# Kernel tuning notes

Measured on AMD Instinct MI355X. Metric: run time of the kernel, lower is better.

## Reference

```python
import jax, jax.numpy as jnp
import numpy as np

NUM_HEADS = 16

def setup_inputs() -> dict:
    key = jax.random.key(0)
    ks = jax.random.split(key, 7)
    B, N, C, R = 2, 2048, 1024, 64
    s = lambda fan_in: 1.0 / np.sqrt(fan_in)
    return {
        "x": jax.random.normal(ks[0], (B, N, C), dtype=jnp.float32),
        "w_qkv_a": jax.random.uniform(ks[1], (C, R), jnp.float32, -s(C), s(C)),
        "w_qkv_b": jax.random.uniform(ks[2], (R, 3 * C), jnp.float32, -s(R), s(R)),
        "w_proj_a": jax.random.uniform(ks[3], (C, R), jnp.float32, -s(C), s(C)),
        "b_proj_a": jax.random.uniform(ks[4], (R,), jnp.float32, -s(C), s(C)),
        "w_proj_b": jax.random.uniform(ks[5], (R, C), jnp.float32, -s(R), s(R)),
        "b_proj_b": jax.random.uniform(ks[6], (C,), jnp.float32, -s(R), s(R)),
    }

def reference(x, w_qkv_a, w_qkv_b, w_proj_a, b_proj_a, w_proj_b, b_proj_b):
    B, N, C = x.shape
    H = NUM_HEADS
    Dh = C // H
    scale = Dh ** -0.5
    # LoRA QKV: dim -> rank -> 3*dim with exact GELU between (no bias, qkv_bias=False)
    qkv = jax.nn.gelu(x @ w_qkv_a, approximate=False) @ w_qkv_b  # [B,N,3C]
    qkv = qkv.reshape(B, N, 3, H, Dh).transpose(2, 0, 3, 1, 4)  # [3,B,H,N,Dh]
    q, k, v = qkv[0] * scale, qkv[1], qkv[2]
    attn = jax.nn.softmax(jnp.einsum("bhqd,bhkd->bhqk", q, k), axis=-1)
    out = jnp.einsum("bhqk,bhkd->bhqd", attn, v)  # [B,H,N,Dh]
    out = out.transpose(0, 2, 1, 3).reshape(B, N, C)
    # LoRA proj: dim -> rank -> dim with bias (proj_bias=True)
    out = jax.nn.gelu(out @ w_proj_a + b_proj_a, approximate=False) @ w_proj_b + b_proj_b
    return out
```

## Files before the change

### kernel.cpp

```cpp
#include <hip/hip_runtime.h>
#include <cstdint>
#include <cstddef>


typedef short short8 __attribute__((ext_vector_type(8)));
typedef float f32x4 __attribute__((ext_vector_type(4)));
typedef __fp16 half2v __attribute__((ext_vector_type(2)));
typedef __fp16 half4 __attribute__((ext_vector_type(4)));

#define MFMA16(a, b, c) __builtin_amdgcn_mfma_f32_16x16x32_bf16((a), (b), (c), 0, 0, 0)
#define MFMA16F(a, b, c) __builtin_amdgcn_mfma_f32_16x16x16f16((a), (b), (c), 0, 0, 0)

#define QSCALE 0.18033688011112042f

__device__ __forceinline__ float fexp2(float x) { return __builtin_amdgcn_exp2f(x); }

__device__ __forceinline__ uint16_t f2b(float f) {
    return (uint16_t)((__float_as_uint(f) + 0x8000u) >> 16);
}
__device__ __forceinline__ uint32_t pkbf(float a, float b) {
    uint32_t ua = __float_as_uint(a) + 0x8000u;
    uint32_t ub = __float_as_uint(b) + 0x8000u;
    return __builtin_amdgcn_perm(ub, ua, 0x07060302);
}
__device__ __forceinline__ uint16_t f2h(float f) {
    half2v t = __builtin_amdgcn_cvt_pkrtz(f, f);
    return __builtin_bit_cast(uint16_t, t[0]);
}
__device__ __forceinline__ float gelu_exact(float x) {
    return 0.5f * x * (1.0f + erff(x * 0.70710678118654752440f));
}
__device__ __forceinline__ short8 ld8(const uint16_t* p) {
    return *reinterpret_cast<const short8*>(p);
}

__global__ __launch_bounds__(256) void prep(const float* __restrict__ x,
                                            const float* __restrict__ wqa,
                                            const float* __restrict__ wqb,
                                            const float* __restrict__ wpa,
                                            const float* __restrict__ wpb,
                                            uint16_t* __restrict__ xb,
                                            uint16_t* __restrict__ wqaT,
                                            uint16_t* __restrict__ wqbT,
                                            uint16_t* __restrict__ wpaT,
                                            uint16_t* __restrict__ wpbT) {
    const int bid = blockIdx.x;
    if (bid < 2048) {
        size_t i = ((size_t)bid * 256 + threadIdx.x) * 8;
        f32x4 a0 = *reinterpret_cast<const f32x4*>(x + i);
        f32x4 a1 = *reinterpret_cast<const f32x4*>(x + i + 4);
        uint32_t* o = reinterpret_cast<uint32_t*>(xb + i);
        o[0] = pkbf(a0[0], a0[1]);
        o[1] = pkbf(a0[2], a0[3]);
        o[2] = pkbf(a1[0], a1[1]);
        o[3] = pkbf(a1[2], a1[3]);
        return;
    }
    int i = (bid - 2048) * 256 + threadIdx.x;
    if (i < 65536) {
        int r = i >> 6, c = i & 63;
        wqaT[(size_t)c * 1024 + r] = f2b(wqa[i]);
    } else if (i < 262144) {
        int j = i - 65536;
        int r = j / 3072, c = j - r * 3072;
        wqbT[(size_t)c * 64 + r] = f2b(wqb[j]);
    } else if (i < 327680) {
        int j = i - 262144;
        int r = j >> 6, c = j & 63;
        wpaT[(size_t)c * 1024 + r] = f2b(wpa[j]);
    } else {
        int j = i - 327680;
        int r = j >> 10, c = j & 1023;
        wpbT[(size_t)c * 64 + r] = f2b(wpb[j]);
    }
}

__global__ __launch_bounds__(512) void rank_gemm(const uint16_t* __restrict__ X,
                                                 const uint16_t* __restrict__ WT,
                                                 const float* __restrict__ bias,
                                                 uint16_t* __restrict__ out) {
    __shared__ float ps[4][16][17];
    const int tid = threadIdx.x;
    const int wave = tid >> 6, lane = tid & 63;
    const int l16 = lane & 15, quad = lane >> 4;
    const int cc = wave & 3, kh = wave >> 2;
    const int rowg = blockIdx.x;

    const uint16_t* ap = X + (size_t)(rowg * 16 + l16) * 1024 + kh * 512 + quad * 8;
    const uint16_t* bp = WT + (size_t)(cc * 16 + l16) * 1024 + kh * 512 + quad * 8;

    f32x4 acc = {0.f, 0.f, 0.f, 0.f};
#pragma unroll 8
    for (int k = 0; k < 16; ++k) {
        acc = MFMA16(ld8(ap + k * 32), ld8(bp + k * 32), acc);
    }

    if (kh == 1) {
#pragma unroll
        for (int r = 0; r < 4; ++r) ps[cc][quad * 4 + r][l16] = acc[r];
    }
    __syncthreads();
    if (kh == 0) {
        const int col = cc * 16 + l16;
        const float bv = bias ? bias[col] : 0.0f;
#pragma unroll
        for (int r = 0; r < 4; ++r) {
            int row = rowg * 16 + quad * 4 + r;
            float v = acc[r] + ps[cc][quad * 4 + r][l16] + bv;
            out[(size_t)row * 64 + col] = f2b(gelu_exact(v));
        }
    }
}

__global__ __launch_bounds__(256) void expand_qkv(const uint16_t* __restrict__ H1,
                                                  const uint16_t* __restrict__ WT,
                                                  uint16_t* __restrict__ Qb,
                                                  uint16_t* __restrict__ Kb,
                                                  uint16_t* __restrict__ Vb) {
    __shared__ __align__(16) uint16_t po[4][16 * 72];
    const int wave = threadIdx.x >> 6;
    const int lane = threadIdx.x & 63;
    const int l16 = lane & 15, quad = lane >> 4;
    const int wg = blockIdx.x * 4 + wave;
    const int rowg = wg / 48;
    const int colg = wg % 48;

    const uint16_t* ap = H1 + (size_t)(rowg * 16 + l16) * 64 + quad * 8;
    const uint16_t* bp = WT + ((size_t)colg * 64 + l16) * 64 + quad * 8;

    f32x4 acc[4];
#pragma unroll
    for (int c = 0; c < 4; ++c) acc[c] = (f32x4){0.f, 0.f, 0.f, 0.f};

#pragma unroll
    for (int i = 0; i < 2; ++i) {
        short8 a = ld8(ap + i * 32);
#pragma unroll
        for (int c = 0; c < 4; ++c) {
            acc[c] = MFMA16(a, ld8(bp + (size_t)c * 16 * 64 + i * 32), acc[c]);
        }
    }

    const int which = colg >> 4;
    const int h = colg & 15;
    uint16_t* pw = po[wave];
#pragma unroll
    for (int c = 0; c < 4; ++c) {
#pragma unroll
        for (int r = 0; r < 4; ++r) {
            float v = acc[c][r];
            uint16_t u = (which == 0) ? f2b(v * QSCALE)
                       : (which == 1) ? f2b(v) : f2h(v);
            pw[(quad * 4 + r) * 72 + c * 16 + l16] = u;
        }
    }
    __builtin_amdgcn_s_waitcnt(0);

    const int grow = rowg * 16 + l16;
    const int b = grow >> 11, n = grow & 2047;
    uint16_t* base = (which == 0) ? Qb : (which == 1) ? Kb : Vb;
    uint16_t* dst = base + ((size_t)(b * 16 + h) * 2048 + n) * 64 + quad * 16;
    *reinterpret_cast<short8*>(dst) = ld8(&pw[l16 * 72 + quad * 16]);
    *reinterpret_cast<short8*>(dst + 8) = ld8(&pw[l16 * 72 + quad * 16 + 8]);
}

__global__ __launch_bounds__(256) void vtrans(const uint16_t* __restrict__ Vb,
                                              uint16_t* __restrict__ Vtb) {
    __shared__ __align__(16) uint16_t tl[64 * 72];
    const int bh = blockIdx.x >> 5;
    const int nt = blockIdx.x & 31;
    const int r = threadIdx.x >> 2;
    const int c0 = (threadIdx.x & 3) << 4;

    const uint16_t* g = Vb + ((size_t)(bh * 2048 + nt * 64 + r)) * 64 + c0;
    union { short8 v; uint16_t u[8]; } a0, a1;
    a0.v = ld8(g);
    a1.v = ld8(g + 8);
#pragma unroll
    for (int j = 0; j < 8; ++j) {
        tl[(c0 + j) * 72 + r] = a0.u[j];
        tl[(c0 + 8 + j) * 72 + r] = a1.u[j];
    }
    __syncthreads();
    uint16_t* o = Vtb + ((size_t)(bh * 64 + r)) * 2048 + nt * 64 + c0;
    *reinterpret_cast<short8*>(o) = ld8(&tl[r * 72 + c0]);
    *reinterpret_cast<short8*>(o + 8) = ld8(&tl[r * 72 + c0 + 8]);
}

__global__ __launch_bounds__(256) void attn_kernel(const uint16_t* __restrict__ Qb,
                                                   const uint16_t* __restrict__ Kb,
                                                   const uint16_t* __restrict__ Vtb,
                                                   uint16_t* __restrict__ AO) {
    __shared__ __align__(16) uint16_t kt[64 * 72];
    __shared__ __align__(16) uint16_t vt[64 * 72];

    const int tid = threadIdx.x;
    const int wave = tid >> 6;
    const int lane = tid & 63;
    const int l16 = lane & 15, quad = lane >> 4;
    const int bh = blockIdx.x >> 5;
    const int qg = blockIdx.x & 31;
    const int q16 = qg * 64 + wave * 16;

    const uint16_t* qp = Qb + ((size_t)(bh * 2048 + q16 + l16)) * 64 + quad * 8;
    const short8 qf0 = ld8(qp);
    const short8 qf1 = ld8(qp + 32);

    f32x4 ot[4];
#pragma unroll
    for (int dc = 0; dc < 4; ++dc) ot[dc] = (f32x4){0.f, 0.f, 0.f, 0.f};
    float lp = 0.f;

    const int sr = tid >> 2;
    const int sc = (tid & 3) << 4;

    for (int t = 0; t < 32; ++t) {
        __syncthreads();
        {
            const uint16_t* kg = Kb + ((size_t)(bh * 2048 + t * 64 + sr)) * 64 + sc;
            *reinterpret_cast<short8*>(&kt[sr * 72 + sc]) = ld8(kg);
            *reinterpret_cast<short8*>(&kt[sr * 72 + sc + 8]) = ld8(kg + 8);
            const uint16_t* vg = Vtb + ((size_t)(bh * 64 + sr)) * 2048 + t * 64 + sc;
            *reinterpret_cast<short8*>(&vt[sr * 72 + sc]) = ld8(vg);
            *reinterpret_cast<short8*>(&vt[sr * 72 + sc + 8]) = ld8(vg + 8);
        }
        __syncthreads();

        half4 pb[4];
#pragma unroll
        for (int kc = 0; kc < 4; ++kc) {
            const uint16_t* kp = &kt[(kc * 16 + l16) * 72 + quad * 8];
            f32x4 st = {0.f, 0.f, 0.f, 0.f};
            st = MFMA16(ld8(kp), qf0, st);
            st = MFMA16(ld8(kp + 32), qf1, st);
            float p0 = fexp2(st[0]), p1 = fexp2(st[1]);
            float p2 = fexp2(st[2]), p3 = fexp2(st[3]);
            lp += (p0 + p1) + (p2 + p3);
            half2v lo = __builtin_amdgcn_cvt_pkrtz(p0, p1);
            half2v hi = __builtin_amdgcn_cvt_pkrtz(p2, p3);
            pb[kc] = __builtin_shufflevector(lo, hi, 0, 1, 2, 3);
        }

#pragma unroll
        for (int dc = 0; dc < 4; ++dc) {
#pragma unroll
            for (int kc = 0; kc < 4; ++kc) {
                const half4 av = *reinterpret_cast<const half4*>(
                    vt + (dc * 16 + l16) * 72 + kc * 16 + quad * 4);
                ot[dc] = MFMA16F(av, pb[kc], ot[dc]);
            }
        }
    }

    lp += __shfl_xor(lp, 16, 64);
    lp += __shfl_xor(lp, 32, 64);
    const float inv = 1.0f / lp;

    __syncthreads();
    uint16_t* pw = &kt[wave * 1152];
#pragma unroll
    for (int dc = 0; dc < 4; ++dc) {
        uint32_t* w = reinterpret_cast<uint32_t*>(&pw[l16 * 72 + dc * 16 + quad * 4]);
        w[0] = pkbf(ot[dc][0] * inv, ot[dc][1] * inv);
        w[1] = pkbf(ot[dc][2] * inv, ot[dc][3] * inv);
    }
    __builtin_amdgcn_s_waitcnt(0);

    const int b = bh >> 4, h = bh & 15;
    const int grow = b * 2048 + q16 + l16;
    uint16_t* dst = AO + (size_t)grow * 1024 + h * 64 + quad * 16;
    *reinterpret_cast<short8*>(dst) = ld8(&pw[l16 * 72 + quad * 16]);
    *reinterpret_cast<short8*>(dst + 8) = ld8(&pw[l16 * 72 + quad * 16 + 8]);
}

__global__ __launch_bounds__(256) void expand_out(const uint16_t* __restrict__ H2,
                                                  const uint16_t* __restrict__ WT,
                                                  const float* __restrict__ bias,
                                                  float* __restrict__ out) {
    const int wave = threadIdx.x >> 6;
    const int lane = threadIdx.x & 63;
    const int l16 = lane & 15, quad = lane >> 4;
    const int wg = blockIdx.x * 4 + wave;
    const int rowg = wg >> 4;
    const int colg = wg & 15;

    const uint16_t* ap = H2 + (size_t)(rowg * 16 + l16) * 64 + quad * 8;
    const uint16_t* bp = WT + ((size_t)colg * 64 + l16) * 64 + quad * 8;

    f32x4 acc[4];
#pragma unroll
    for (int c = 0; c < 4; ++c) acc[c] = (f32x4){0.f, 0.f, 0.f, 0.f};

#pragma unroll
    for (int i = 0; i < 2; ++i) {
        short8 a = ld8(ap + i * 32);
#pragma unroll
        for (int c = 0; c < 4; ++c) {
            acc[c] = MFMA16(a, ld8(bp + (size_t)c * 16 * 64 + i * 32), acc[c]);
        }
    }

#pragma unroll
    for (int c = 0; c < 4; ++c) {
        int col = colg * 64 + c * 16 + l16;
        float bv = bias[col];
#pragma unroll
        for (int r = 0; r < 4; ++r) {
            int row = rowg * 16 + quad * 4 + r;
            out[(size_t)row * 1024 + col] = acc[c][r] + bv;
        }
    }
}

extern "C" void kernel_launch(void* const* d_in, const int* in_sizes, int n_in,
                              void* d_out, int out_size, void* d_ws, size_t ws_size,
                              hipStream_t stream) {
    const float* x   = (const float*)d_in[0];
    const float* wqa = (const float*)d_in[1];
    const float* wqb = (const float*)d_in[2];
    const float* wpa = (const float*)d_in[3];
    const float* bpa = (const float*)d_in[4];
    const float* wpb = (const float*)d_in[5];
    const float* bpb = (const float*)d_in[6];
    float* out = (float*)d_out;
    uint16_t* ws = (uint16_t*)d_ws;

    uint16_t* wqaT = ws + 0;
    uint16_t* wqbT = ws + 65536;
    uint16_t* wpaT = ws + 262144;
    uint16_t* wpbT = ws + 327680;
    uint16_t* h1   = ws + 393216;
    uint16_t* Qb   = ws + 655360;
    uint16_t* Kb   = ws + 4849664;
    uint16_t* xb   = Kb;
    uint16_t* Vtb  = ws + 9043968;
    uint16_t* AO   = ws + 13238272;
    uint16_t* Vb   = AO;
    uint16_t* h2   = ws + 17432576;
    (void)in_sizes; (void)n_in; (void)out_size; (void)ws_size;

    prep<<<3584, 256, 0, stream>>>(x, wqa, wqb, wpa, wpb, xb, wqaT, wqbT, wpaT, wpbT);
    rank_gemm<<<256, 512, 0, stream>>>(xb, wqaT, nullptr, h1);
    expand_qkv<<<3072, 256, 0, stream>>>(h1, wqbT, Qb, Kb, Vb);
    vtrans<<<1024, 256, 0, stream>>>(Vb, Vtb);
    attn_kernel<<<1024, 256, 0, stream>>>(Qb, Kb, Vtb, AO);
    rank_gemm<<<256, 512, 0, stream>>>(AO, wpaT, bpa, h2);
    expand_out<<<1024, 256, 0, stream>>>(h2, wpbT, bpb, out);
}
```

Baseline: 205.2 us.

## Fuse V transpose into QKV expand, read K/V directly, fuse projection GEMMs

The V transpose kernel is removed: expand_qkv now computes V^T by swapping the MFMA operands and writes it straight into the transposed layout with scalar strided stores. The attention kernel drops LDS staging and the per-tile barriers for K and V, loading MFMA fragments directly from global memory and relying on cache reuse across waves. The two projection kernels are merged into one, which keeps the rank-64 GELU activation in LDS. This removes two launches and intermediate round trips, at the risk of uncoalesced 2-byte V stores and redundant global loads of K and V in attention.

```diff
diff --git a/kernel.cpp b/kernel.cpp
--- a/kernel.cpp
+++ b/kernel.cpp
@@ -77,7 +77,6 @@
 
 __global__ __launch_bounds__(512) void rank_gemm(const uint16_t* __restrict__ X,
                                                  const uint16_t* __restrict__ WT,
-                                                 const float* __restrict__ bias,
                                                  uint16_t* __restrict__ out) {
     __shared__ float ps[4][16][17];
     const int tid = threadIdx.x;
@@ -102,11 +101,10 @@
     __syncthreads();
     if (kh == 0) {
         const int col = cc * 16 + l16;
-        const float bv = bias ? bias[col] : 0.0f;
 #pragma unroll
         for (int r = 0; r < 4; ++r) {
             int row = rowg * 16 + quad * 4 + r;
-            float v = acc[r] + ps[cc][quad * 4 + r][l16] + bv;
+            float v = acc[r] + ps[cc][quad * 4 + r][l16];
             out[(size_t)row * 64 + col] = f2b(gelu_exact(v));
         }
     }
@@ -116,7 +114,7 @@
                                                   const uint16_t* __restrict__ WT,
                                                   uint16_t* __restrict__ Qb,
                                                   uint16_t* __restrict__ Kb,
-                                                  uint16_t* __restrict__ Vb) {
+                                                  uint16_t* __restrict__ Vtb) {
     __shared__ __align__(16) uint16_t po[4][16 * 72];
     const int wave = threadIdx.x >> 6;
     const int lane = threadIdx.x & 63;
@@ -128,71 +126,69 @@
     const uint16_t* ap = H1 + (size_t)(rowg * 16 + l16) * 64 + quad * 8;
     const uint16_t* bp = WT + ((size_t)colg * 64 + l16) * 64 + quad * 8;
 
-    f32x4 acc[4];
-#pragma unroll
-    for (int c = 0; c < 4; ++c) acc[c] = (f32x4){0.f, 0.f, 0.f, 0.f};
-
-#pragma unroll
-    for (int i = 0; i < 2; ++i) {
-        short8 a = ld8(ap + i * 32);
-#pragma unroll
-        for (int c = 0; c < 4; ++c) {
-            acc[c] = MFMA16(a, ld8(bp + (size_t)c * 16 * 64 + i * 32), acc[c]);
-        }
-    }
-
     const int which = colg >> 4;
     const int h = colg & 15;
-    uint16_t* pw = po[wave];
-#pragma unroll
-    for (int c = 0; c < 4; ++c) {
-#pragma unroll
-        for (int r = 0; r < 4; ++r) {
-            float v = acc[c][r];
-            uint16_t u = (which == 0) ? f2b(v * QSCALE)
-                       : (which == 1) ? f2b(v) : f2h(v);
-            pw[(quad * 4 + r) * 72 + c * 16 + l16] = u;
-        }
-    }
-    __builtin_amdgcn_s_waitcnt(0);
-
-    const int grow = rowg * 16 + l16;
-    const int b = grow >> 11, n = grow & 2047;
-    uint16_t* base = (which == 0) ? Qb : (which == 1) ? Kb : Vb;
-    uint16_t* dst = base + ((size_t)(b * 16 + h) * 2048 + n) * 64 + quad * 16;
-    *reinterpret_cast<short8*>(dst) = ld8(&pw[l16 * 72 + quad * 16]);
-    *reinterpret_cast<short8*>(dst + 8) = ld8(&pw[l16 * 72 + quad * 16 + 8]);
-}
-
-__global__ __launch_bounds__(256) void vtrans(const uint16_t* __restrict__ Vb,
-                                              uint16_t* __restrict__ Vtb) {
-    __shared__ __align__(16) uint16_t tl[64 * 72];
-    const int bh = blockIdx.x >> 5;
-    const int nt = blockIdx.x & 31;
-    const int r = threadIdx.x >> 2;
-    const int c0 = (threadIdx.x & 3) << 4;
-
-    const uint16_t* g = Vb + ((size_t)(bh * 2048 + nt * 64 + r)) * 64 + c0;
-    union { short8 v; uint16_t u[8]; } a0, a1;
-    a0.v = ld8(g);
-    a1.v = ld8(g + 8);
-#pragma unroll
-    for (int j = 0; j < 8; ++j) {
-        tl[(c0 + j) * 72 + r] = a0.u[j];
-        tl[(c0 + 8 + j) * 72 + r] = a1.u[j];
-    }
-    __syncthreads();
-    uint16_t* o = Vtb + ((size_t)(bh * 64 + r)) * 2048 + nt * 64 + c0;
-    *reinterpret_cast<short8*>(o) = ld8(&tl[r * 72 + c0]);
-    *reinterpret_cast<short8*>(o + 8) = ld8(&tl[r * 72 + c0 + 8]);
+
+    f32x4 acc[4];
+#pragma unroll
+    for (int c = 0; c < 4; ++c) acc[c] = (f32x4){0.f, 0.f, 0.f, 0.f};
+
+    if (which < 2) {
+#pragma unroll
+        for (int i = 0; i < 2; ++i) {
+            short8 a = ld8(ap + i * 32);
+#pragma unroll
+            for (int c = 0; c < 4; ++c) {
+                acc[c] = MFMA16(a, ld8(bp + (size_t)c * 1024 + i * 32), acc[c]);
+            }
+        }
+        uint16_t* pw = po[wave];
+#pragma unroll
+        for (int c = 0; c < 4; ++c) {
+#pragma unroll
+            for (int r = 0; r < 4; ++r) {
+                float v = acc[c][r];
+                uint16_t u = (which == 0) ? f2b(v * QSCALE) : f2b(v);
+                pw[(quad * 4 + r) * 72 + c * 16 + l16] = u;
+            }
+        }
+        __builtin_amdgcn_s_waitcnt(0);
+
+        const int grow = rowg * 16 + l16;
+        const int b = grow >> 11, n = grow & 2047;
+        uint16_t* base = (which == 0) ? Qb : Kb;
+        uint16_t* dst = base + ((size_t)(b * 16 + h) * 2048 + n) * 64 + quad * 16;
+        *reinterpret_cast<short8*>(dst) = ld8(&pw[l16 * 72 + quad * 16]);
+        *reinterpret_cast<short8*>(dst + 8) = ld8(&pw[l16 * 72 + quad * 16 + 8]);
+    } else {
+#pragma unroll
+        for (int i = 0; i < 2; ++i) {
+            short8 a = ld8(ap + i * 32);
+#pragma unroll
+            for (int c = 0; c < 4; ++c) {
+                acc[c] = MFMA16(ld8(bp + (size_t)c * 1024 + i * 32), a, acc[c]);
+            }
+        }
+        const int grow = rowg * 16 + l16;
+        const int b = grow >> 11, n = grow & 2047;
+        uint16_t* vb = Vtb + (size_t)(b * 16 + h) * 64 * 2048 + n;
+#pragma unroll
+        for (int c = 0; c < 4; ++c) {
+#pragma unroll
+            for (int r = 0; r < 4; ++r) {
+                int d = c * 16 + quad * 4 + r;
+                vb[(size_t)d * 2048] = f2h(acc[c][r]);
+            }
+            vb += 0;
+        }
+    }
 }
 
 __global__ __launch_bounds__(256) void attn_kernel(const uint16_t* __restrict__ Qb,
                                                    const uint16_t* __restrict__ Kb,
                                                    const uint16_t* __restrict__ Vtb,
                                                    uint16_t* __restrict__ AO) {
-    __shared__ __align__(16) uint16_t kt[64 * 72];
-    __shared__ __align__(16) uint16_t vt[64 * 72];
+    __shared__ __align__(16) uint16_t pws[4][16 * 72];
 
     const int tid = threadIdx.x;
     const int wave = tid >> 6;
@@ -206,30 +202,19 @@
     const short8 qf0 = ld8(qp);
     const short8 qf1 = ld8(qp + 32);
 
+    const uint16_t* kbase = Kb + (size_t)bh * 2048 * 64 + (size_t)l16 * 64 + quad * 8;
+    const uint16_t* vbase = Vtb + (size_t)bh * 64 * 2048 + (size_t)l16 * 2048 + quad * 4;
+
     f32x4 ot[4];
 #pragma unroll
     for (int dc = 0; dc < 4; ++dc) ot[dc] = (f32x4){0.f, 0.f, 0.f, 0.f};
     float lp = 0.f;
 
-    const int sr = tid >> 2;
-    const int sc = (tid & 3) << 4;
-
     for (int t = 0; t < 32; ++t) {
-        __syncthreads();
-        {
-            const uint16_t* kg = Kb + ((size_t)(bh * 2048 + t * 64 + sr)) * 64 + sc;
-            *reinterpret_cast<short8*>(&kt[sr * 72 + sc]) = ld8(kg);
-            *reinterpret_cast<short8*>(&kt[sr * 72 + sc + 8]) = ld8(kg + 8);
-            const uint16_t* vg = Vtb + ((size_t)(bh * 64 + sr)) * 2048 + t * 64 + sc;
-            *reinterpret_cast<short8*>(&vt[sr * 72 + sc]) = ld8(vg);
-            *reinterpret_cast<short8*>(&vt[sr * 72 + sc + 8]) = ld8(vg + 8);
-        }
-        __syncthreads();
-
         half4 pb[4];
 #pragma unroll
         for (int kc = 0; kc < 4; ++kc) {
-            const uint16_t* kp = &kt[(kc * 16 + l16) * 72 + quad * 8];
+            const uint16_t* kp = kbase + (size_t)(t * 64 + kc * 16) * 64;
             f32x4 st = {0.f, 0.f, 0.f, 0.f};
             st = MFMA16(ld8(kp), qf0, st);
             st = MFMA16(ld8(kp + 32), qf1, st);
@@ -243,10 +228,10 @@
 
 #pragma unroll
         for (int dc = 0; dc < 4; ++dc) {
+            const uint16_t* vp = vbase + (size_t)dc * 16 * 2048 + t * 64;
 #pragma unroll
             for (int kc = 0; kc < 4; ++kc) {
-                const half4 av = *reinterpret_cast<const half4*>(
-                    vt + (dc * 16 + l16) * 72 + kc * 16 + quad * 4);
+                const half4 av = *reinterpret_cast<const half4*>(vp + kc * 16);
                 ot[dc] = MFMA16F(av, pb[kc], ot[dc]);
             }
         }
@@ -256,8 +241,7 @@
     lp += __shfl_xor(lp, 32, 64);
     const float inv = 1.0f / lp;
 
-    __syncthreads();
-    uint16_t* pw = &kt[wave * 1152];
+    uint16_t* pw = pws[wave];
 #pragma unroll
     for (int dc = 0; dc < 4; ++dc) {
         uint32_t* w = reinterpret_cast<uint32_t*>(&pw[l16 * 72 + dc * 16 + quad * 4]);
@@ -273,41 +257,59 @@
     *reinterpret_cast<short8*>(dst + 8) = ld8(&pw[l16 * 72 + quad * 16 + 8]);
 }
 
-__global__ __launch_bounds__(256) void expand_out(const uint16_t* __restrict__ H2,
-                                                  const uint16_t* __restrict__ WT,
-                                                  const float* __restrict__ bias,
+__global__ __launch_bounds__(512) void proj_fused(const uint16_t* __restrict__ AO,
+                                                  const uint16_t* __restrict__ wpaT,
+                                                  const float* __restrict__ bpa,
+                                                  const uint16_t* __restrict__ wpbT,
+                                                  const float* __restrict__ bpb,
                                                   float* __restrict__ out) {
-    const int wave = threadIdx.x >> 6;
-    const int lane = threadIdx.x & 63;
+    __shared__ float ps[4][16][17];
+    __shared__ __align__(16) uint16_t h2L[16 * 72];
+    const int tid = threadIdx.x;
+    const int wave = tid >> 6, lane = tid & 63;
     const int l16 = lane & 15, quad = lane >> 4;
-    const int wg = blockIdx.x * 4 + wave;
-    const int rowg = wg >> 4;
-    const int colg = wg & 15;
-
-    const uint16_t* ap = H2 + (size_t)(rowg * 16 + l16) * 64 + quad * 8;
-    const uint16_t* bp = WT + ((size_t)colg * 64 + l16) * 64 + quad * 8;
-
-    f32x4 acc[4];
-#pragma unroll
-    for (int c = 0; c < 4; ++c) acc[c] = (f32x4){0.f, 0.f, 0.f, 0.f};
-
-#pragma unroll
-    for (int i = 0; i < 2; ++i) {
-        short8 a = ld8(ap + i * 32);
-#pragma unroll
-        for (int c = 0; c < 4; ++c) {
-            acc[c] = MFMA16(a, ld8(bp + (size_t)c * 16 * 64 + i * 32), acc[c]);
-        }
-    }
-
-#pragma unroll
-    for (int c = 0; c < 4; ++c) {
-        int col = colg * 64 + c * 16 + l16;
-        float bv = bias[col];
+    const int cc = wave & 3, kh = wave >> 2;
+    const int rowg = blockIdx.x;
+
+    {
+        const uint16_t* ap = AO + (size_t)(rowg * 16 + l16) * 1024 + kh * 512 + quad * 8;
+        const uint16_t* bp = wpaT + (size_t)(cc * 16 + l16) * 1024 + kh * 512 + quad * 8;
+        f32x4 acc = {0.f, 0.f, 0.f, 0.f};
+#pragma unroll 8
+        for (int k = 0; k < 16; ++k) {
+            acc = MFMA16(ld8(ap + k * 32), ld8(bp + k * 32), acc);
+        }
+        if (kh == 1) {
+#pragma unroll
+            for (int r = 0; r < 4; ++r) ps[cc][quad * 4 + r][l16] = acc[r];
+        }
+        __syncthreads();
+        if (kh == 0) {
+            const int col = cc * 16 + l16;
+            const float bv = bpa[col];
+#pragma unroll
+            for (int r = 0; r < 4; ++r) {
+                float v = acc[r] + ps[cc][quad * 4 + r][l16] + bv;
+                h2L[(quad * 4 + r) * 72 + col] = f2b(gelu_exact(v));
+            }
+        }
+        __syncthreads();
+    }
+
+    const short8 a0 = ld8(&h2L[l16 * 72 + quad * 8]);
+    const short8 a1 = ld8(&h2L[l16 * 72 + 32 + quad * 8]);
+#pragma unroll
+    for (int i = 0; i < 8; ++i) {
+        const int col0 = (wave * 8 + i) * 16;
+        const uint16_t* bp = wpbT + (size_t)(col0 + l16) * 64 + quad * 8;
+        f32x4 acc = {0.f, 0.f, 0.f, 0.f};
+        acc = MFMA16(a0, ld8(bp), acc);
+        acc = MFMA16(a1, ld8(bp + 32), acc);
+        const float bv = bpb[col0 + l16];
 #pragma unroll
         for (int r = 0; r < 4; ++r) {
             int row = rowg * 16 + quad * 4 + r;
-            out[(size_t)row * 1024 + col] = acc[c][r] + bv;
+            out[(size_t)row * 1024 + col0 + l16] = acc[r] + bv;
         }
     }
 }
@@ -335,15 +337,11 @@
     uint16_t* xb   = Kb;
     uint16_t* Vtb  = ws + 9043968;
     uint16_t* AO   = ws + 13238272;
-    uint16_t* Vb   = AO;
-    uint16_t* h2   = ws + 17432576;
     (void)in_sizes; (void)n_in; (void)out_size; (void)ws_size;
 
     prep<<<3584, 256, 0, stream>>>(x, wqa, wqb, wpa, wpb, xb, wqaT, wqbT, wpaT, wpbT);
-    rank_gemm<<<256, 512, 0, stream>>>(xb, wqaT, nullptr, h1);
-    expand_qkv<<<3072, 256, 0, stream>>>(h1, wqbT, Qb, Kb, Vb);
-    vtrans<<<1024, 256, 0, stream>>>(Vb, Vtb);
+    rank_gemm<<<256, 512, 0, stream>>>(xb, wqaT, h1);
+    expand_qkv<<<3072, 256, 0, stream>>>(h1, wqbT, Qb, Kb, Vtb);
     attn_kernel<<<1024, 256, 0, stream>>>(Qb, Kb, Vtb, AO);
-    rank_gemm<<<256, 512, 0, stream>>>(AO, wpaT, bpa, h2);
-    expand_out<<<1024, 256, 0, stream>>>(h2, wpbT, bpb, out);
-}
+    proj_fused<<<256, 512, 0, stream>>>(AO, wpaT, bpa, wpbT, bpb, out);
+}
```

Measured after the change: 462.9 us. 126% more time.
